# Performance work log

Measured on AMD Instinct MI355X. Metric: run time of the kernel, lower is better.

## Reference

```python
import jax, jax.numpy as jnp
import numpy as np

BN_EPS = 1e-5


def conv3x3(x, w):
    # 3x3 'same' conv, stride 1, no bias (matches nn.Conv2d(k=3, padding=1, bias=False))
    return jax.lax.conv_general_dilated(
        x, w, window_strides=(1, 1), padding='SAME',
        dimension_numbers=('NCHW', 'OIHW', 'NCHW'))


def batchnorm(x, gamma, beta, mean, var):
    # eval-mode BatchNorm2d with running stats
    scale = (gamma / jnp.sqrt(var + BN_EPS))[None, :, None, None]
    return (x - mean[None, :, None, None]) * scale + beta[None, :, None, None]


def setup_inputs() -> dict:
    key = jax.random.key(0)
    ks = jax.random.split(key, 13)
    B, C, H, W = 16, 64, 160, 160
    wshape = (C, C, 3, 3)
    inp = {
        'x': jax.random.normal(ks[0], (B, C, H, W), jnp.float32),
        'w_cv1': jax.random.normal(ks[1], wshape, jnp.float32) * 0.05,
        'g1': jax.random.uniform(ks[2], (C,), jnp.float32, 0.5, 1.5),
        'b1': jax.random.normal(ks[3], (C,), jnp.float32) * 0.1,
        'm1': jax.random.normal(ks[4], (C,), jnp.float32) * 0.1,
        'v1': jax.random.uniform(ks[5], (C,), jnp.float32, 0.5, 1.5),
        'wq': jax.random.normal(ks[6], wshape, jnp.float32) * 0.05,
        'wk': jax.random.normal(ks[7], wshape, jnp.float32) * 0.05,
        'wv': jax.random.normal(ks[8], wshape, jnp.float32) * 0.05,
        'g2': jax.random.uniform(ks[9], (C,), jnp.float32, 0.5, 1.5),
        'b2': jax.random.normal(ks[10], (C,), jnp.float32) * 0.1,
        'm2': jax.random.normal(ks[11], (C,), jnp.float32) * 0.1,
        'v2': jax.random.uniform(ks[12], (C,), jnp.float32, 0.5, 1.5),
    }
    return inp


def reference(x, w_cv1, g1, b1, m1, v1, wq, wk, wv, g2, b2, m2, v2):
    # cv1: Conv -> BN -> SiLU
    y = jax.nn.silu(batchnorm(conv3x3(x, w_cv1), g1, b1, m1, v1))

    # CSA_ConvBlock on y (c_ channels)
    fq = conv3x3(y, wq)   # [B,C,H,W]
    fk = conv3x3(y, wk)
    fv = conv3x3(y, wv)
    H, W = y.shape[2], y.shape[3]

    # Original: f_sim[b,i,j,h1,h2] = sum_w fq[b,i,h1,w]*fk[b,j,h2,w] / sqrt(W);
    # then sum over j, then mean-ish sum over (h1,h2)/H^2 -> f_scores[b,i].
    # Algebraically identical reorder (sum-before-matmul):
    k_sum = fk.sum(axis=(1, 2))                       # [B,W], sum over channels j and rows h2
    scale = 1.0 / (float(W) ** 0.5 * float(H) * float(H))
    f_scores = jnp.einsum('bchw,bw->bc', fq, k_sum) * scale  # [B,C]
    scores = jax.nn.softmax(f_scores, axis=1)[:, :, None, None]

    r = scores * fv + y
    r = jax.nn.relu(batchnorm(r, g2, b2, m2, v2))

    # shortcut: c1 == c2 and shortcut=True
    return x + r
```

## Files before the change

kernel.cpp:

```cpp
#include <hip/hip_runtime.h>
#include <hip/hip_bf16.h>
#include <math.h>

#define NB 16
#define NC 64
#define NH 160
#define NW 160

typedef __attribute__((ext_vector_type(8))) short bf16x8;
typedef __attribute__((ext_vector_type(4))) float f32x4;
typedef __attribute__((ext_vector_type(8))) unsigned short u16x8;
typedef __attribute__((ext_vector_type(4))) unsigned short u16x4;

__device__ __forceinline__ unsigned short f2bf(float v) {
  union { __hip_bfloat16 b; unsigned short u; } cv; cv.b = __float2bfloat16(v); return cv.u;
}
__device__ __forceinline__ float bf2f(unsigned short u) {
  union { unsigned u; float f; } cv; cv.u = ((unsigned)u) << 16; return cv.f;
}

__global__ void pack_w_kernel3(const float* __restrict__ wA, const float* __restrict__ wB,
                               const float* __restrict__ wq, const float* __restrict__ wk,
                               unsigned short* __restrict__ apkA, unsigned short* __restrict__ apkB,
                               float* __restrict__ wqt, float* __restrict__ wkst) {
  int idx = blockIdx.x * 256 + threadIdx.x;
  if (idx < 2 * 36864) {
    const float* w = (idx < 36864) ? wA : wB;
    unsigned short* apk = (idx < 36864) ? apkA : apkB;
    int i = (idx < 36864) ? idx : idx - 36864;
    int j = i & 7, l = (i >> 3) & 63, rest = i >> 9;
    int ks = rest % 18, ct = rest / 18;
    int cih = ks & 1, tap = ks >> 1, kh = tap / 3, kw = tap % 3;
    int co = ct * 16 + (l & 15), ci = cih * 32 + (l >> 4) * 8 + j;
    apk[i] = f2bf(w[(((size_t)co * NC + ci) * 3 + kh) * 3 + kw]);
  } else if (idx < 3 * 36864) {
    int i2 = idx - 2 * 36864;
    int c = i2 & 63, tau = i2 >> 6;
    int i = tau & 63, jj = tau >> 6;
    wqt[i2] = wq[(size_t)c * 576 + i * 9 + jj];
  } else if (idx < 3 * 36864 + 576) {
    int i3 = idx - 3 * 36864;
    int i = i3 & 63, jj = i3 >> 6;
    float s = 0.f;
    for (int cj = 0; cj < NC; ++cj) s += wk[(size_t)cj * 576 + i * 9 + jj];
    wkst[i3] = s;
  }
}

__global__ __launch_bounds__(256) void to_nhwc(const float* __restrict__ x,
                                               unsigned short* __restrict__ xt) {
  __shared__ unsigned short l[64 * 162];
  int bh = blockIdx.x; int b = bh / NH, h = bh % NH;
  for (int i = threadIdx.x; i < 64 * NW; i += 256) {
    int ci = i / NW, w = i % NW;
    l[ci * 162 + w] = f2bf(x[(((size_t)b * NC + ci) * NH + h) * NW + w]);
  }
  __syncthreads();
  unsigned short* o = xt + ((size_t)b * NH + h) * NW * NC;
  for (int i = threadIdx.x; i < NW * 8; i += 256) {
    int w = i >> 3, s = i & 7;
    u16x8 v;
#pragma unroll
    for (int j = 0; j < 8; ++j) v[j] = l[(s * 8 + j) * 162 + w];
    *(u16x8*)&o[w * 64 + s * 8] = v;
  }
}

template<bool FINAL>
__global__ __launch_bounds__(256, 2) void conv3x3_mfma5(
    const unsigned short* __restrict__ in_nhwc, const unsigned short* __restrict__ apk,
    const float* __restrict__ gg, const float* __restrict__ bbeta,
    const float* __restrict__ mmean, const float* __restrict__ vvar,
    void* __restrict__ outv, const float* __restrict__ scores,
    const float* __restrict__ xres)
{
  __shared__ unsigned short ring[6 * 34 * 64];
  __shared__ unsigned short epi[FINAL ? 8 : 2 * 32 * 72];

  const int t = threadIdx.x, lane = t & 63, wave = t >> 6;
  const int q = lane >> 4, col = lane & 15;

  int g = blockIdx.x;
  int sw = (g & 7) * 160 + (g >> 3);
  const int b = sw / 80;
  int rem = sw % 80;
  const int h0 = (rem / 5) * 10, w0 = (rem % 5) * 32;

  float scR[4], shR[4], scoR[4];
#pragma unroll
  for (int r = 0; r < 4; ++r) {
    int co = wave * 16 + q * 4 + r;
    float s = gg[co] * rsqrtf(vvar[co] + 1e-5f);
    scR[r] = s; shR[r] = bbeta[co] - mmean[co] * s;
    scoR[r] = FINAL ? scores[b * NC + co] : 0.f;
  }

  bf16x8 wf[18];
#pragma unroll
  for (int ks = 0; ks < 18; ++ks)
    wf[ks] = *(const bf16x8*)&apk[((size_t)(wave * 18 + ks) * 64 + lane) * 8];

  const unsigned short* inb = in_nhwc + (size_t)b * NH * NW * 64;

#define SLOT(R) ((int)((unsigned)((R) + 1) % 6u) * 2176)
#define STG_ISSUE(ROW, V0, V1, A0, A1)                                        \
  { int row_ = (ROW);                                                         \
    bool rowok_ = (unsigned)row_ < (unsigned)NH;                              \
    int slot_ = SLOT(row_);                                                   \
    { int wcc = t >> 3, s8 = t & 7; int wsrc = w0 + wcc - 1;                  \
      A0 = slot_ + wcc * 64 + ((s8 ^ (wcc & 7)) << 3);                        \
      V0 = (u16x8){};                                                         \
      if (rowok_ && (unsigned)wsrc < (unsigned)NW)                            \
        V0 = *(const u16x8*)&inb[((size_t)row_ * NW + wsrc) * 64 + s8 * 8];   \
    }                                                                         \
    if (t < 16) { int c = 256 + t; int wcc = c >> 3, s8 = c & 7;              \
      int wsrc = w0 + wcc - 1;                                                \
      A1 = slot_ + wcc * 64 + ((s8 ^ (wcc & 7)) << 3);                        \
      V1 = (u16x8){};                                                         \
      if (rowok_ && (unsigned)wsrc < (unsigned)NW)                            \
        V1 = *(const u16x8*)&inb[((size_t)row_ * NW + wsrc) * 64 + s8 * 8];   \
    } }
#define STG_COMMIT(V0, V1, A0, A1)                                            \
  *(u16x8*)&ring[A0] = V0;                                                    \
  if (t < 16) *(u16x8*)&ring[A1] = V1;

  for (int rr = -1; rr <= 2; ++rr) {
    u16x8 v0, v1 = {}; int a0, a1 = 0;
    STG_ISSUE(h0 + rr, v0, v1, a0, a1)
    STG_COMMIT(v0, v1, a0, a1)
  }
  __syncthreads();

  for (int wi = 0; wi < 5; ++wi) {
    const int h = h0 + wi * 2;
    u16x8 va0, va1 = {}, vb0, vb1 = {}; int aa0, aa1 = 0, ab0, ab1 = 0;
    const bool doS = (wi < 4);
    if (doS) {
      STG_ISSUE(h + 3, va0, va1, aa0, aa1)
      STG_ISSUE(h + 4, vb0, vb1, ab0, ab1)
    }

    const int sl[4] = { SLOT(h - 1), SLOT(h), SLOT(h + 1), SLOT(h + 2) };
    f32x4 acc[2][2];
#pragma unroll
    for (int o = 0; o < 2; ++o) { acc[o][0] = (f32x4){0,0,0,0}; acc[o][1] = (f32x4){0,0,0,0}; }

#pragma unroll
    for (int ri = 0; ri < 4; ++ri) {
#pragma unroll
      for (int kw = 0; kw < 3; ++kw) {
#pragma unroll
        for (int cih = 0; cih < 2; ++cih) {
          const int wcb = col + kw;
          const int ea = sl[ri] + wcb * 64 + (((cih << 2) + q) ^ (wcb & 7)) * 8;
          const bf16x8* bp = (const bf16x8*)&ring[ea];
          bf16x8 B0 = bp[0], B1 = bp[128];
          if (ri <= 2) {
            const int ks = (ri * 3 + kw) * 2 + cih;
            acc[0][0] = __builtin_amdgcn_mfma_f32_16x16x32_bf16(wf[ks], B0, acc[0][0], 0, 0, 0);
            acc[0][1] = __builtin_amdgcn_mfma_f32_16x16x32_bf16(wf[ks], B1, acc[0][1], 0, 0, 0);
          }
          if (ri >= 1) {
            const int ks = ((ri - 1) * 3 + kw) * 2 + cih;
            acc[1][0] = __builtin_amdgcn_mfma_f32_16x16x32_bf16(wf[ks], B0, acc[1][0], 0, 0, 0);
            acc[1][1] = __builtin_amdgcn_mfma_f32_16x16x32_bf16(wf[ks], B1, acc[1][1], 0, 0, 0);
          }
        }
      }
    }

    if constexpr (!FINAL) {
#pragma unroll
      for (int o = 0; o < 2; ++o) {
#pragma unroll
        for (int wt = 0; wt < 2; ++wt) {
          u16x4 ev;
#pragma unroll
          for (int r = 0; r < 4; ++r) {
            float z = scR[r] * acc[o][wt][r] + shR[r];
            ev[r] = f2bf(z / (1.f + __expf(-z)));
          }
          *(u16x4*)&epi[((o * 32) + wt * 16 + col) * 72 + wave * 16 + q * 4] = ev;
        }
      }
      if (doS) { STG_COMMIT(va0, va1, aa0, aa1) STG_COMMIT(vb0, vb1, ab0, ab1) }
      __syncthreads();
      { int w = t >> 3, s = t & 7;
#pragma unroll
        for (int o = 0; o < 2; ++o) {
          unsigned short* yo = (unsigned short*)outv + (((size_t)b * NH + h + o) * NW + w0) * 64;
          *(u16x8*)&yo[w * 64 + s * 8] = *(const u16x8*)&epi[((o * 32) + w) * 72 + s * 8];
        }
      }
      __syncthreads();
    } else {
      if (doS) { STG_COMMIT(va0, va1, aa0, aa1) STG_COMMIT(vb0, vb1, ab0, ab1) }
      float* outp = (float*)outv;
#pragma unroll
      for (int o = 0; o < 2; ++o) {
        const int rb1 = sl[1 + o];
#pragma unroll
        for (int wt = 0; wt < 2; ++wt) {
          int wcc = wt * 16 + col + 1;
          int gr = (wave * 2 + (q >> 1)) ^ (wcc & 7);
          u16x4 yv = *(const u16x4*)&ring[rb1 + wcc * 64 + gr * 8 + (q & 1) * 4];
#pragma unroll
          for (int r = 0; r < 4; ++r) {
            int co = wave * 16 + q * 4 + r;
            float rv = scoR[r] * acc[o][wt][r] + bf2f(yv[r]);
            float rb_ = scR[r] * rv + shR[r];
            rb_ = fmaxf(rb_, 0.f);
            size_t oi = (((size_t)b * NC + co) * NH + h + o) * NW + w0 + wt * 16 + col;
            outp[oi] = xres[oi] + rb_;
          }
        }
      }
      __syncthreads();
    }
  }
#undef STG_ISSUE
#undef STG_COMMIT
#undef SLOT
}

__global__ void colsum_kernel(const unsigned short* __restrict__ y, float* __restrict__ ycol) {
  int id = blockIdx.x * 256 + threadIdx.x;
  if (id >= NB * NW * NC) return;
  int c = id & 63, bw = id >> 6;
  int w = bw % NW, b = bw / NW;
  float s = 0.f;
  for (int h = 0; h < NH; ++h)
    s += bf2f(y[(((size_t)b * NH + h) * NW + w) * 64 + c]);
  ycol[id] = s;
}

__device__ __forceinline__ float zval(const float* __restrict__ ycol,
                                      const unsigned short* __restrict__ y,
                                      int b, int i, int kh, int wp) {
  float z = ycol[((size_t)b * NW + wp) * 64 + i];
  if (kh == 0) z -= bf2f(y[(((size_t)b * NH + (NH - 1)) * NW + wp) * 64 + i]);
  if (kh == 2) z -= bf2f(y[(((size_t)b * NH) * NW + wp) * 64 + i]);
  return z;
}

__global__ __launch_bounds__(256) void ks_kernel(
    const float* __restrict__ ycol, const unsigned short* __restrict__ y,
    const float* __restrict__ wkst, float* __restrict__ ks)
{
  int id = blockIdx.x * 4 + (threadIdx.x >> 6);
  int lane = threadIdx.x & 63;
  int b = id / NW, w = id % NW;
  float s = 0.f;
#pragma unroll
  for (int jj = 0; jj < 9; ++jj) {
    int kh = jj / 3, kw = jj % 3;
    int wp = w + kw - 1;
    if ((unsigned)wp < (unsigned)NW)
      s += wkst[jj * 64 + lane] * zval(ycol, y, b, lane, kh, wp);
  }
#pragma unroll
  for (int off = 32; off; off >>= 1) s += __shfl_xor(s, off);
  if (lane == 0) ks[id] = s;
}

__global__ __launch_bounds__(256) void u_kernel(
    const float* __restrict__ ycol, const unsigned short* __restrict__ y,
    const float* __restrict__ ks, float* __restrict__ U)
{
  __shared__ float red[4][64];
  int bid = blockIdx.x;
  int b = bid / 9, jj = bid % 9;
  int kh = jj / 3, kw = jj % 3;
  int i = threadIdx.x & 63, ch = threadIdx.x >> 6;
  float s = 0.f;
  for (int w = ch * 40; w < ch * 40 + 40; ++w) {
    int wp = w + kw - 1;
    if ((unsigned)wp < (unsigned)NW)
      s += zval(ycol, y, b, i, kh, wp) * ks[b * NW + w];
  }
  red[ch][i] = s;
  __syncthreads();
  if (threadIdx.x < 64)
    U[((size_t)b * 9 + jj) * 64 + threadIdx.x] =
        red[0][threadIdx.x] + red[1][threadIdx.x] + red[2][threadIdx.x] + red[3][threadIdx.x];
}

__global__ __launch_bounds__(256) void scores_kernel2(
    const float* __restrict__ wqt, const float* __restrict__ U,
    float* __restrict__ scores)
{
  __shared__ float red[4][64];
  int b = blockIdx.x;
  int c = threadIdx.x & 63, p = threadIdx.x >> 6;
  const float* Ub = U + (size_t)b * 576;
  float s = 0.f;
  for (int tau = p * 144; tau < p * 144 + 144; ++tau)
    s += wqt[(size_t)tau * 64 + c] * Ub[tau];
  red[p][c] = s;
  __syncthreads();
  if (threadIdx.x < 64) {
    const float scale = 1.0f / (sqrtf((float)NW) * (float)NH * (float)NH);
    float f = (red[0][c] + red[1][c] + red[2][c] + red[3][c]) * scale;
    float mx = f;
#pragma unroll
    for (int off = 32; off; off >>= 1) mx = fmaxf(mx, __shfl_xor(mx, off));
    float e = __expf(f - mx);
    float sm = e;
#pragma unroll
    for (int off = 32; off; off >>= 1) sm += __shfl_xor(sm, off);
    scores[b * NC + c] = e / sm;
  }
}

extern "C" void kernel_launch(void* const* d_in, const int* in_sizes, int n_in,
                              void* d_out, int out_size, void* d_ws, size_t ws_size,
                              hipStream_t stream) {
  const float* x  = (const float*)d_in[0];
  const float* w1 = (const float*)d_in[1];
  const float* g1 = (const float*)d_in[2];
  const float* b1 = (const float*)d_in[3];
  const float* m1 = (const float*)d_in[4];
  const float* v1 = (const float*)d_in[5];
  const float* wq = (const float*)d_in[6];
  const float* wk = (const float*)d_in[7];
  const float* wv = (const float*)d_in[8];
  const float* g2 = (const float*)d_in[9];
  const float* b2 = (const float*)d_in[10];
  const float* m2 = (const float*)d_in[11];
  const float* v2 = (const float*)d_in[12];
  float* out = (float*)d_out;

  unsigned short* apk1 = (unsigned short*)d_ws;
  unsigned short* apk2 = apk1 + 36864;
  float* wqt  = (float*)(apk2 + 36864);
  float* wkst = wqt + 36864;
  float* ycol = wkst + 576;
  float* ks   = ycol + NB * NW * NC;
  float* U    = ks + NB * NW;
  float* scr  = U + NB * 576;
  unsigned short* xt = (unsigned short*)(scr + 1024);
  unsigned short* y  = xt + (size_t)NB * NH * NW * 64;

  pack_w_kernel3<<<dim3(435), 256, 0, stream>>>(w1, wv, wq, wk, apk1, apk2, wqt, wkst);
  to_nhwc<<<dim3(NB * NH), 256, 0, stream>>>(x, xt);

  conv3x3_mfma5<false><<<dim3(1280), 256, 0, stream>>>(
      xt, apk1, g1, b1, m1, v1, (void*)y, nullptr, nullptr);

  colsum_kernel<<<dim3((NB * NW * NC + 255) / 256), 256, 0, stream>>>(y, ycol);
  ks_kernel<<<dim3(NB * NW / 4), 256, 0, stream>>>(ycol, y, wkst, ks);
  u_kernel<<<dim3(NB * 9), 256, 0, stream>>>(ycol, y, ks, U);
  scores_kernel2<<<dim3(NB), 256, 0, stream>>>(wqt, U, scr);

  conv3x3_mfma5<true><<<dim3(1280), 256, 0, stream>>>(
      y, apk2, g2, b2, m2, v2, (void*)out, scr, x);
}
```

Before: 186.1 us.

## Fuse column-sum of y into first conv epilogue and raise final conv occupancy

The first conv kernel now accumulates per-strip column sums of its bf16 SiLU output in shared memory and writes partial sums per 10-row strip. A small kernel then reduces the 16 strips per column, replacing the old pass that reread all of y over 160 rows. The final conv also gets launch bounds of 3 blocks per SIMD, which may limit registers and cause spills. Extra LDS (8KB) in the first conv could reduce its occupancy.

```diff
diff --git a/kernel.cpp b/kernel.cpp
--- a/kernel.cpp
+++ b/kernel.cpp
@@ -67,15 +67,16 @@
 }
 
 template<bool FINAL>
-__global__ __launch_bounds__(256, 2) void conv3x3_mfma5(
+__global__ __launch_bounds__(256, FINAL ? 3 : 2) void conv3x3_mfma6(
     const unsigned short* __restrict__ in_nhwc, const unsigned short* __restrict__ apk,
     const float* __restrict__ gg, const float* __restrict__ bbeta,
     const float* __restrict__ mmean, const float* __restrict__ vvar,
     void* __restrict__ outv, const float* __restrict__ scores,
-    const float* __restrict__ xres)
+    const float* __restrict__ xres, float* __restrict__ colpart)
 {
   __shared__ unsigned short ring[6 * 34 * 64];
   __shared__ unsigned short epi[FINAL ? 8 : 2 * 32 * 72];
+  __shared__ f32x4 csv[FINAL ? 1 : 512];
 
   const int t = threadIdx.x, lane = t & 63, wave = t >> 6;
   const int q = lane >> 4, col = lane & 15;
@@ -124,6 +125,10 @@
   *(u16x8*)&ring[A0] = V0;                                                    \
   if (t < 16) *(u16x8*)&ring[A1] = V1;
 
+  if constexpr (!FINAL) {
+    csv[t] = (f32x4){0.f, 0.f, 0.f, 0.f};
+    csv[t + 256] = (f32x4){0.f, 0.f, 0.f, 0.f};
+  }
   for (int rr = -1; rr <= 2; ++rr) {
     u16x8 v0, v1 = {}; int a0, a1 = 0;
     STG_ISSUE(h0 + rr, v0, v1, a0, a1)
@@ -170,6 +175,8 @@
     }
 
     if constexpr (!FINAL) {
+      f32x4 csadd[2];
+      csadd[0] = (f32x4){0,0,0,0}; csadd[1] = (f32x4){0,0,0,0};
 #pragma unroll
       for (int o = 0; o < 2; ++o) {
 #pragma unroll
@@ -181,8 +188,13 @@
             ev[r] = f2bf(z / (1.f + __expf(-z)));
           }
           *(u16x4*)&epi[((o * 32) + wt * 16 + col) * 72 + wave * 16 + q * 4] = ev;
+#pragma unroll
+          for (int r = 0; r < 4; ++r) csadd[wt][r] += bf2f(ev[r]);
         }
       }
+      { int cc = wave * 4 + q;
+        csv[cc * 32 + col]      += csadd[0];
+        csv[cc * 32 + 16 + col] += csadd[1]; }
       if (doS) { STG_COMMIT(va0, va1, aa0, aa1) STG_COMMIT(vb0, vb1, ab0, ab1) }
       __syncthreads();
       { int w = t >> 3, s = t & 7;
@@ -218,19 +230,27 @@
       __syncthreads();
     }
   }
+
+  if constexpr (!FINAL) {
+    const int strip = h0 / 10;
+    float* pp = colpart + (((size_t)b * 16 + strip) * NW + w0) * 64;
+    int w = t >> 3, g0 = t & 7;
+    *(f32x4*)&pp[w * 64 + g0 * 4]       = csv[g0 * 32 + w];
+    *(f32x4*)&pp[w * 64 + (g0 + 8) * 4] = csv[(g0 + 8) * 32 + w];
+  }
 #undef STG_ISSUE
 #undef STG_COMMIT
 #undef SLOT
 }
 
-__global__ void colsum_kernel(const unsigned short* __restrict__ y, float* __restrict__ ycol) {
+__global__ void colsum2_kernel(const float* __restrict__ part, float* __restrict__ ycol) {
   int id = blockIdx.x * 256 + threadIdx.x;
   if (id >= NB * NW * NC) return;
-  int c = id & 63, bw = id >> 6;
-  int w = bw % NW, b = bw / NW;
+  int c = id & 63; int bw = id >> 6; int w = bw % NW; int b = bw / NW;
+  const float* p = part + (((size_t)b * 16) * NW + w) * 64 + c;
   float s = 0.f;
-  for (int h = 0; h < NH; ++h)
-    s += bf2f(y[(((size_t)b * NH + h) * NW + w) * 64 + c]);
+#pragma unroll
+  for (int st = 0; st < 16; ++st) s += p[(size_t)st * NW * 64];
   ycol[id] = s;
 }
 
@@ -338,20 +358,21 @@
   float* ks   = ycol + NB * NW * NC;
   float* U    = ks + NB * NW;
   float* scr  = U + NB * 576;
-  unsigned short* xt = (unsigned short*)(scr + 1024);
+  float* part = scr + 1024;
+  unsigned short* xt = (unsigned short*)(part + (size_t)NB * 16 * NW * 64);
   unsigned short* y  = xt + (size_t)NB * NH * NW * 64;
 
   pack_w_kernel3<<<dim3(435), 256, 0, stream>>>(w1, wv, wq, wk, apk1, apk2, wqt, wkst);
   to_nhwc<<<dim3(NB * NH), 256, 0, stream>>>(x, xt);
 
-  conv3x3_mfma5<false><<<dim3(1280), 256, 0, stream>>>(
-      xt, apk1, g1, b1, m1, v1, (void*)y, nullptr, nullptr);
-
-  colsum_kernel<<<dim3((NB * NW * NC + 255) / 256), 256, 0, stream>>>(y, ycol);
+  conv3x3_mfma6<false><<<dim3(1280), 256, 0, stream>>>(
+      xt, apk1, g1, b1, m1, v1, (void*)y, nullptr, nullptr, part);
+
+  colsum2_kernel<<<dim3((NB * NW * NC + 255) / 256), 256, 0, stream>>>(part, ycol);
   ks_kernel<<<dim3(NB * NW / 4), 256, 0, stream>>>(ycol, y, wkst, ks);
   u_kernel<<<dim3(NB * 9), 256, 0, stream>>>(ycol, y, ks, U);
   scores_kernel2<<<dim3(NB), 256, 0, stream>>>(wqt, U, scr);
 
-  conv3x3_mfma5<true><<<dim3(1280), 256, 0, stream>>>(
-      y, apk2, g2, b2, m2, v2, (void*)out, scr, x);
-}
+  conv3x3_mfma6<true><<<dim3(1280), 256, 0, stream>>>(
+      y, apk2, g2, b2, m2, v2, (void*)out, scr, x, nullptr);
+}
```

After: 183.7 us. About the same (-1.3%).
